# Performance work log

Hardware: AMD Instinct MI355X
Metric: run time of the kernel (lower is better)

The kernel has to match this reference:

```python
import jax, jax.numpy as jnp
import numpy as np

B, S, D = 32, 512, 768
H = 12
HD = D // H
SCALE = HD ** -0.5


def setup_inputs() -> dict:
    key = jax.random.key(0)
    ks = jax.random.split(key, 5)
    return {
        "x": jax.random.normal(ks[0], (B, S, D), dtype=jnp.float32),
        "qkv_w": jax.random.normal(ks[1], (3 * D, D), dtype=jnp.float32) * (D ** -0.5),
        "qkv_b": jax.random.normal(ks[2], (3 * D,), dtype=jnp.float32) * 0.02,
        "proj_w": jax.random.normal(ks[3], (D, D), dtype=jnp.float32) * (D ** -0.5),
        "proj_b": jax.random.normal(ks[4], (D,), dtype=jnp.float32) * 0.02,
    }


def reference(x, qkv_w, qkv_b, proj_w, proj_b) -> jnp.ndarray:
    b, s, d = x.shape
    # fused QKV projection (torch Linear: x @ W.T + b)
    qkv = x @ qkv_w.T + qkv_b                      # [B,S,3D]
    qkv = qkv.reshape(b, s, 3, H, HD)
    qkv = jnp.transpose(qkv, (2, 0, 3, 1, 4))      # [3,B,H,S,HD]
    q, k, v = qkv[0], qkv[1], qkv[2]
    scores = jnp.einsum("bhqd,bhkd->bhqk", q, k) * SCALE  # [B,H,S,S]
    # attn_drop with p=0.0 (eval) -> identity
    attn = jax.nn.softmax(scores, axis=-1)
    out = jnp.einsum("bhqk,bhkd->bhqd", attn, v)   # [B,H,S,HD]
    out = jnp.transpose(out, (0, 2, 1, 3)).reshape(b, s, d)
    out = out @ proj_w.T + proj_b                  # proj_drop p=0.0 -> identity
    return out
```

## Files before the change

kernel.cpp:

```cpp
#include <hip/hip_runtime.h>
#include <hip/hip_bf16.h>

#define B_  32
#define S_  512
#define D_  768
#define H_  12
#define HD_ 64
#define QKV_ELEMS (B_ * H_ * S_ * HD_)

typedef __hip_bfloat16 bf16;
typedef short bf16x8_t __attribute__((ext_vector_type(8)));
typedef float f32x4_t  __attribute__((ext_vector_type(4)));

__device__ __forceinline__ float bf2f(bf16 x) { return __bfloat162float(x); }
__device__ __forceinline__ bf16  f2bf(float x) { return __float2bfloat16(x); }

__device__ __forceinline__ void gl_lds16(const short* g, short* l) {
    __builtin_amdgcn_global_load_lds(
        (const __attribute__((address_space(1))) void*)g,
        (__attribute__((address_space(3))) void*)l, 16, 0, 0);
}

__global__ __launch_bounds__(256) void f2bf3_kernel(
    const float* __restrict__ in0, unsigned short* __restrict__ out0, int n0,
    const float* __restrict__ in1, unsigned short* __restrict__ out1, int n1,
    const float* __restrict__ in2, unsigned short* __restrict__ out2, int n2)
{
    int i = blockIdx.x * 256 + threadIdx.x;
    const float* in; unsigned short* out;
    if (i < n0)           { in = in0; out = out0; }
    else if (i < n0 + n1) { in = in1; out = out1; i -= n0; }
    else                  { in = in2; out = out2; i -= n0 + n1;
                            if (i >= n2) return; }
    float4 v = reinterpret_cast<const float4*>(in)[i];
    ushort4 o;
    o.x = __bfloat16_as_ushort(f2bf(v.x));
    o.y = __bfloat16_as_ushort(f2bf(v.y));
    o.z = __bfloat16_as_ushort(f2bf(v.z));
    o.w = __bfloat16_as_ushort(f2bf(v.w));
    reinterpret_cast<ushort4*>(out)[i] = o;
}

#define GEMM_CORE(As, Bs, Aptr, Bptr, m0, n0, K)                               \
    const int t = threadIdx.x;                                                 \
    const int w = t >> 6, lane = t & 63;                                       \
    const int wr = w >> 1, wc = w & 1;                                         \
    const int quad = lane >> 4, l16 = lane & 15;                               \
    f32x4_t acc[4][4] = {};                                                    \
    const int lrow = lane >> 3;                                                \
    const int scol = (((lane & 7) ^ (lrow & 7)) * 8);                          \
    _Pragma("unroll")                                                          \
    for (int j = 0; j < 4; ++j) {                                              \
        int R = j * 32 + w * 8;                                                \
        gl_lds16((Aptr) + (size_t)((m0) + R + lrow) * (K) + scol, &(As)[R * 64]); \
        gl_lds16((Bptr) + (size_t)((n0) + R + lrow) * (K) + scol, &(Bs)[R * 64]); \
    }                                                                          \
    for (int k0 = 0; k0 < (K); k0 += 64) {                                     \
        __syncthreads();           \
        _Pragma("unroll")                                                      \
        for (int ks = 0; ks < 64; ks += 32) {                                  \
            bf16x8_t af[4], bf_[4];                                            \
            _Pragma("unroll")                                                  \
            for (int tm = 0; tm < 4; ++tm)                                     \
                af[tm] = *(const bf16x8_t*)&(As)[(wr * 64 + tm * 16 + l16) * 64 \
                        + ((((ks >> 3) + quad) ^ (l16 & 7)) * 8)];             \
            _Pragma("unroll")                                                  \
            for (int tn = 0; tn < 4; ++tn)                                     \
                bf_[tn] = *(const bf16x8_t*)&(Bs)[(wc * 64 + tn * 16 + l16) * 64 \
                        + ((((ks >> 3) + quad) ^ (l16 & 7)) * 8)];             \
            _Pragma("unroll")                                                  \
            for (int tm = 0; tm < 4; ++tm)                                     \
                _Pragma("unroll")                                              \
                for (int tn = 0; tn < 4; ++tn)                                 \
                    acc[tm][tn] = __builtin_amdgcn_mfma_f32_16x16x32_bf16(     \
                        af[tm], bf_[tn], acc[tm][tn], 0, 0, 0);                \
        }                                                                      \
        __syncthreads();                   \
        if (k0 + 64 < (K)) {                                                   \
            _Pragma("unroll")                                                  \
            for (int j = 0; j < 4; ++j) {                                      \
                int R = j * 32 + w * 8;                                        \
                gl_lds16((Aptr) + (size_t)((m0) + R + lrow) * (K) + k0 + 64 + scol, \
                         &(As)[R * 64]);                                       \
                gl_lds16((Bptr) + (size_t)((n0) + R + lrow) * (K) + k0 + 64 + scol, \
                         &(Bs)[R * 64]);                                       \
            }                                                                  \
        }                                                                      \
    }

__global__ __launch_bounds__(256, 4) void qkv_gemm_mfma(
    const short* __restrict__ A, const short* __restrict__ W,
    const float* __restrict__ bias,
    bf16* __restrict__ Q, bf16* __restrict__ Kp, bf16* __restrict__ Vp)
{
    __shared__ short As[128 * 64];
    __shared__ short Bs[128 * 64];
    const int bid = blockIdx.x;
    const int swz = (bid & 7) * (2304 / 8) + (bid >> 3);
    const int n0 = (swz % 18) * 128;
    const int m0 = (swz / 18) * 128;
    GEMM_CORE(As, Bs, A, W, m0, n0, 768)

    const int which = n0 / 768;
    const int h = ((n0 + wc * 64) % 768) >> 6;
    bf16* dst = (which == 0) ? Q : (which == 1) ? Kp : Vp;
    float bv[4];
#pragma unroll
    for (int tn = 0; tn < 4; ++tn) bv[tn] = bias[n0 + wc * 64 + tn * 16 + l16];
#pragma unroll
    for (int tm = 0; tm < 4; ++tm) {
#pragma unroll
        for (int r = 0; r < 4; ++r) {
            int m = m0 + wr * 64 + tm * 16 + quad * 4 + r;
            int b = m >> 9, s = m & 511;
            size_t rb = (((size_t)b * H_ + h) * S_ + s) * HD_;
#pragma unroll
            for (int tn = 0; tn < 4; ++tn)
                dst[rb + tn * 16 + l16] = f2bf(acc[tm][tn][r] + bv[tn]);
        }
    }
}

__global__ __launch_bounds__(256, 4) void proj_gemm_mfma(
    const short* __restrict__ A, const short* __restrict__ W,
    const float* __restrict__ bias, float* __restrict__ out)
{
    __shared__ short As[128 * 64];
    __shared__ short Bs[128 * 64];
    const int bid = blockIdx.x;
    const int swz = (bid & 7) * (768 / 8) + (bid >> 3);
    const int n0 = (swz % 6) * 128;
    const int m0 = (swz / 6) * 128;
    GEMM_CORE(As, Bs, A, W, m0, n0, 768)

    float bv[4];
#pragma unroll
    for (int tn = 0; tn < 4; ++tn) bv[tn] = bias[n0 + wc * 64 + tn * 16 + l16];
#pragma unroll
    for (int tm = 0; tm < 4; ++tm) {
#pragma unroll
        for (int r = 0; r < 4; ++r) {
            int m = m0 + wr * 64 + tm * 16 + quad * 4 + r;
#pragma unroll
            for (int tn = 0; tn < 4; ++tn)
                out[(size_t)m * 768 + n0 + wc * 64 + tn * 16 + l16] =
                    acc[tm][tn][r] + bv[tn];
        }
    }
}

#define QT 128
#define KT 64
#define PS 68
#define VS 68

__global__ __launch_bounds__(256, 3) void attn_mfma(
    const short* __restrict__ Qg, const short* __restrict__ Kg,
    const short* __restrict__ Vg, bf16* __restrict__ O)
{
    __shared__ short Ks[2][KT * 64];
    __shared__ short Vt[2][64 * VS];
    __shared__ short Ps[QT * PS];

    const int t = threadIdx.x;
    const int w = t >> 6, lane = t & 63;
    const int quad = lane >> 4, l16 = lane & 15;
    const int lrow = lane >> 3;
    const int scol = (((lane & 7) ^ (lrow & 7)) * 8);
    const int bid = blockIdx.x;
    const int bh = (bid & 7) + 8 * (bid >> 5);
    const int qt = (bid >> 3) & 3;
    const int q0 = qt * QT;
    const size_t base = (size_t)bh * (S_ * HD_);
    const int wq = w * 32;

    bf16x8_t aq[2][2];
#pragma unroll
    for (int tm = 0; tm < 2; ++tm)
#pragma unroll
        for (int ksi = 0; ksi < 2; ++ksi)
            aq[tm][ksi] = *(const bf16x8_t*)(Qg + base
                + (size_t)(q0 + wq + tm * 16 + l16) * 64 + ksi * 32 + quad * 8);

    f32x4_t Oacc[2][4] = {};
    float lsum[2][4] = {};

#pragma unroll
    for (int j = 0; j < 2; ++j) {
        int R = j * 32 + w * 8;
        gl_lds16(Kg + base + (size_t)(R + lrow) * 64 + scol, &Ks[0][R * 64]);
    }
    {
        const bf16x8_t* gv = (const bf16x8_t*)(Vg + base + (size_t)lane * 64 + w * 16);
        bf16x8_t v0 = gv[0], v1 = gv[1];
#pragma unroll
        for (int i = 0; i < 8; ++i) {
            Vt[0][(w * 16 + i) * VS + lane]     = v0[i];
            Vt[0][(w * 16 + 8 + i) * VS + lane] = v1[i];
        }
    }
    __syncthreads();

    for (int kt = 0; kt < 8; ++kt) {
        const int cur = kt & 1, nxt = cur ^ 1;
        bf16x8_t pv0 = {}, pv1 = {};
        if (kt < 7) {
#pragma unroll
            for (int j = 0; j < 2; ++j) {
                int R = j * 32 + w * 8;
                gl_lds16(Kg + base + (size_t)((kt + 1) * KT + R + lrow) * 64 + scol,
                         &Ks[nxt][R * 64]);
            }
            const bf16x8_t* gv = (const bf16x8_t*)(Vg + base
                + (size_t)((kt + 1) * KT + lane) * 64 + w * 16);
            pv0 = gv[0]; pv1 = gv[1];
        }

        f32x4_t sc[2][4] = {};
        __builtin_amdgcn_s_setprio(1);
#pragma unroll
        for (int ks = 0; ks < 64; ks += 32) {
            bf16x8_t bk[4];
#pragma unroll
            for (int tn = 0; tn < 4; ++tn)
                bk[tn] = *(const bf16x8_t*)&Ks[cur][(tn * 16 + l16) * 64
                        + ((((ks >> 3) + quad) ^ (l16 & 7)) * 8)];
#pragma unroll
            for (int tm = 0; tm < 2; ++tm)
#pragma unroll
                for (int tn = 0; tn < 4; ++tn)
                    sc[tm][tn] = __builtin_amdgcn_mfma_f32_16x16x32_bf16(
                        aq[tm][ks >> 5], bk[tn], sc[tm][tn], 0, 0, 0);
        }
        __builtin_amdgcn_s_setprio(0);

#pragma unroll
        for (int tm = 0; tm < 2; ++tm) {
#pragma unroll
            for (int r = 0; r < 4; ++r) {
                int row = wq + tm * 16 + quad * 4 + r;
                float rs = 0.f;
#pragma unroll
                for (int tn = 0; tn < 4; ++tn) {
                    float p = __expf(sc[tm][tn][r] * 0.125f);
                    rs += p;
                    Ps[row * PS + tn * 16 + l16] = (short)__bfloat16_as_ushort(f2bf(p));
                }
                lsum[tm][r] += rs;
            }
        }

        __builtin_amdgcn_s_setprio(1);
#pragma unroll
        for (int ks = 0; ks < 64; ks += 32) {
            bf16x8_t ap[2], bv[4];
#pragma unroll
            for (int tm = 0; tm < 2; ++tm)
                ap[tm] = *(const bf16x8_t*)&Ps[(wq + tm * 16 + l16) * PS + ks + quad * 8];
#pragma unroll
            for (int tn = 0; tn < 4; ++tn)
                bv[tn] = *(const bf16x8_t*)&Vt[cur][(tn * 16 + l16) * VS + ks + quad * 8];
#pragma unroll
            for (int tm = 0; tm < 2; ++tm)
#pragma unroll
                for (int tn = 0; tn < 4; ++tn)
                    Oacc[tm][tn] = __builtin_amdgcn_mfma_f32_16x16x32_bf16(
                        ap[tm], bv[tn], Oacc[tm][tn], 0, 0, 0);
        }
        __builtin_amdgcn_s_setprio(0);

        if (kt < 7) {
#pragma unroll
            for (int i = 0; i < 8; ++i) {
                Vt[nxt][(w * 16 + i) * VS + lane]     = pv0[i];
                Vt[nxt][(w * 16 + 8 + i) * VS + lane] = pv1[i];
            }
        }
        __syncthreads();
    }

    float linv[2][4];
#pragma unroll
    for (int tm = 0; tm < 2; ++tm)
#pragma unroll
        for (int r = 0; r < 4; ++r) {
            float v = lsum[tm][r];
            v += __shfl_xor(v, 1, 64);
            v += __shfl_xor(v, 2, 64);
            v += __shfl_xor(v, 4, 64);
            v += __shfl_xor(v, 8, 64);
            linv[tm][r] = 1.f / v;
        }
    const int b = bh / H_, h = bh % H_;
#pragma unroll
    for (int tm = 0; tm < 2; ++tm) {
#pragma unroll
        for (int r = 0; r < 4; ++r) {
            int row = q0 + wq + tm * 16 + quad * 4 + r;
            size_t ob = ((size_t)b * S_ + row) * D_ + h * HD_;
#pragma unroll
            for (int tn = 0; tn < 4; ++tn)
                O[ob + tn * 16 + l16] = f2bf(Oacc[tm][tn][r] * linv[tm][r]);
        }
    }
}

extern "C" void kernel_launch(void* const* d_in, const int* in_sizes, int n_in,
                              void* d_out, int out_size, void* d_ws, size_t ws_size,
                              hipStream_t stream) {
    const float* x      = (const float*)d_in[0];
    const float* qkv_w  = (const float*)d_in[1];
    const float* qkv_b  = (const float*)d_in[2];
    const float* proj_w = (const float*)d_in[3];
    const float* proj_b = (const float*)d_in[4];
    float* out = (float*)d_out;

    unsigned short* q     = (unsigned short*)d_ws;
    unsigned short* k     = q + QKV_ELEMS;
    unsigned short* v     = k + QKV_ELEMS;
    unsigned short* slot4 = v + QKV_ELEMS;
    unsigned short* wq    = slot4 + QKV_ELEMS;
    unsigned short* wp    = wq + 2304 * 768;

    const int nx = 16384 * 768 / 4, nw1 = 2304 * 768 / 4, nw2 = 768 * 768 / 4;
    f2bf3_kernel<<<(nx + nw1 + nw2 + 255) / 256, 256, 0, stream>>>(
        x, slot4, nx, qkv_w, wq, nw1, proj_w, wp, nw2);

    qkv_gemm_mfma<<<dim3(2304), 256, 0, stream>>>(
        (const short*)slot4, (const short*)wq, qkv_b,
        (bf16*)q, (bf16*)k, (bf16*)v);

    attn_mfma<<<dim3(32 * 12 * 4), 256, 0, stream>>>(
        (const short*)q, (const short*)k, (const short*)v, (bf16*)slot4);

    proj_gemm_mfma<<<dim3(768), 256, 0, stream>>>(
        (const short*)slot4, (const short*)wp, proj_b, out);
}
```

Baseline: 245.3 us.

## Load GEMM weight fragments straight into registers with one-step prefetch, dropping B LDS tile

The shared GEMM core no longer stages the weight (B) tile through LDS. Each wave now loads its B fragments from global memory directly into registers and prefetches the next k-slice while computing the current one. This halves LDS usage and removes the B LDS reads and writes. In exchange each 64-column wave pair re-reads the same weights from global or L2 without sharing, and register pressure rises under launch_bounds(256,4).

```diff
diff --git a/kernel.cpp b/kernel.cpp
--- a/kernel.cpp
+++ b/kernel.cpp
@@ -41,7 +41,7 @@
     reinterpret_cast<ushort4*>(out)[i] = o;
 }
 
-#define GEMM_CORE(As, Bs, Aptr, Bptr, m0, n0, K)                               \
+#define GEMM_CORE(As, Aptr, Bptr, m0, n0, K)                                   \
     const int t = threadIdx.x;                                                 \
     const int w = t >> 6, lane = t & 63;                                       \
     const int wr = w >> 1, wc = w & 1;                                         \
@@ -49,42 +49,60 @@
     f32x4_t acc[4][4] = {};                                                    \
     const int lrow = lane >> 3;                                                \
     const int scol = (((lane & 7) ^ (lrow & 7)) * 8);                          \
+    const short* Bp[4];                                                        \
+    _Pragma("unroll")                                                          \
+    for (int tn = 0; tn < 4; ++tn)                                             \
+        Bp[tn] = (Bptr) + (size_t)((n0) + wc * 64 + tn * 16 + l16) * (K)       \
+                 + quad * 8;                                                   \
     _Pragma("unroll")                                                          \
     for (int j = 0; j < 4; ++j) {                                              \
         int R = j * 32 + w * 8;                                                \
         gl_lds16((Aptr) + (size_t)((m0) + R + lrow) * (K) + scol, &(As)[R * 64]); \
-        gl_lds16((Bptr) + (size_t)((n0) + R + lrow) * (K) + scol, &(Bs)[R * 64]); \
     }                                                                          \
+    bf16x8_t bcur[4][2];                                                       \
+    _Pragma("unroll")                                                          \
+    for (int tn = 0; tn < 4; ++tn)                                             \
+        _Pragma("unroll")                                                      \
+        for (int ks = 0; ks < 2; ++ks)                                         \
+            bcur[tn][ks] = *(const bf16x8_t*)(Bp[tn] + ks * 32);               \
+    _Pragma("unroll")                                                          \
     for (int k0 = 0; k0 < (K); k0 += 64) {                                     \
-        __syncthreads();           \
+        __syncthreads();              \
+        bf16x8_t bnxt[4][2];                                                   \
+        if (k0 + 64 < (K)) {                                                   \
+            _Pragma("unroll")                                                  \
+            for (int tn = 0; tn < 4; ++tn)                                     \
+                _Pragma("unroll")                                              \
+                for (int ks = 0; ks < 2; ++ks)                                 \
+                    bnxt[tn][ks] = *(const bf16x8_t*)(Bp[tn] + k0 + 64 + ks * 32); \
+        }                                                                      \
         _Pragma("unroll")                                                      \
-        for (int ks = 0; ks < 64; ks += 32) {                                  \
-            bf16x8_t af[4], bf_[4];                                            \
+        for (int ks = 0; ks < 2; ++ks) {                                       \
+            bf16x8_t af[4];                                                    \
             _Pragma("unroll")                                                  \
             for (int tm = 0; tm < 4; ++tm)                                     \
                 af[tm] = *(const bf16x8_t*)&(As)[(wr * 64 + tm * 16 + l16) * 64 \
-                        + ((((ks >> 3) + quad) ^ (l16 & 7)) * 8)];             \
-            _Pragma("unroll")                                                  \
-            for (int tn = 0; tn < 4; ++tn)                                     \
-                bf_[tn] = *(const bf16x8_t*)&(Bs)[(wc * 64 + tn * 16 + l16) * 64 \
-                        + ((((ks >> 3) + quad) ^ (l16 & 7)) * 8)];             \
+                        + (((ks * 4 + quad) ^ (l16 & 7)) * 8)];                \
             _Pragma("unroll")                                                  \
             for (int tm = 0; tm < 4; ++tm)                                     \
                 _Pragma("unroll")                                              \
                 for (int tn = 0; tn < 4; ++tn)                                 \
                     acc[tm][tn] = __builtin_amdgcn_mfma_f32_16x16x32_bf16(     \
-                        af[tm], bf_[tn], acc[tm][tn], 0, 0, 0);                \
+                        af[tm], bcur[tn][ks], acc[tm][tn], 0, 0, 0);           \
         }                                                                      \
-        __syncthreads();                   \
+        __syncthreads();           \
         if (k0 + 64 < (K)) {                                                   \
             _Pragma("unroll")                                                  \
             for (int j = 0; j < 4; ++j) {                                      \
                 int R = j * 32 + w * 8;                                        \
                 gl_lds16((Aptr) + (size_t)((m0) + R + lrow) * (K) + k0 + 64 + scol, \
                          &(As)[R * 64]);                                       \
-                gl_lds16((Bptr) + (size_t)((n0) + R + lrow) * (K) + k0 + 64 + scol, \
-                         &(Bs)[R * 64]);                                       \
             }                                                                  \
+            _Pragma("unroll")                                                  \
+            for (int tn = 0; tn < 4; ++tn)                                     \
+                _Pragma("unroll")                                              \
+                for (int ks = 0; ks < 2; ++ks)                                 \
+                    bcur[tn][ks] = bnxt[tn][ks];                               \
         }                                                                      \
     }
 
@@ -94,12 +112,11 @@
     bf16* __restrict__ Q, bf16* __restrict__ Kp, bf16* __restrict__ Vp)
 {
     __shared__ short As[128 * 64];
-    __shared__ short Bs[128 * 64];
     const int bid = blockIdx.x;
     const int swz = (bid & 7) * (2304 / 8) + (bid >> 3);
     const int n0 = (swz % 18) * 128;
     const int m0 = (swz / 18) * 128;
-    GEMM_CORE(As, Bs, A, W, m0, n0, 768)
+    GEMM_CORE(As, A, W, m0, n0, 768)
 
     const int which = n0 / 768;
     const int h = ((n0 + wc * 64) % 768) >> 6;
@@ -126,12 +143,11 @@
     const float* __restrict__ bias, float* __restrict__ out)
 {
     __shared__ short As[128 * 64];
-    __shared__ short Bs[128 * 64];
     const int bid = blockIdx.x;
     const int swz = (bid & 7) * (768 / 8) + (bid >> 3);
     const int n0 = (swz % 6) * 128;
     const int m0 = (swz / 6) * 128;
-    GEMM_CORE(As, Bs, A, W, m0, n0, 768)
+    GEMM_CORE(As, A, W, m0, n0, 768)
 
     float bv[4];
 #pragma unroll
```

Result: slower. 329.1 us (+34.2%).

## Split attention block into 8 waves with 16 query rows each

Applied to the files above, without the earlier changes.

The attention kernel now launches 512 threads per block, and each of 8 waves owns 16 query rows instead of 32, which halves the per-wave accumulators and Q fragments. K/V tile loading is redistributed so each wave loads 8 rows of K and an 8-column slice of V. The aim is lower register pressure and more resident waves to hide latency. In exchange, each K/V LDS fragment is reused across fewer MFMAs per wave, and block-wide syncs now involve more waves.

```diff
diff --git a/kernel.cpp b/kernel.cpp
--- a/kernel.cpp
+++ b/kernel.cpp
@@ -154,7 +154,7 @@
 #define PS 68
 #define VS 68
 
-__global__ __launch_bounds__(256, 3) void attn_mfma(
+__global__ __launch_bounds__(512, 4) void attn_mfma(
     const short* __restrict__ Qg, const short* __restrict__ Kg,
     const short* __restrict__ Vg, bf16* __restrict__ O)
 {
@@ -172,51 +172,37 @@
     const int qt = (bid >> 3) & 3;
     const int q0 = qt * QT;
     const size_t base = (size_t)bh * (S_ * HD_);
-    const int wq = w * 32;
-
-    bf16x8_t aq[2][2];
-#pragma unroll
-    for (int tm = 0; tm < 2; ++tm)
-#pragma unroll
-        for (int ksi = 0; ksi < 2; ++ksi)
-            aq[tm][ksi] = *(const bf16x8_t*)(Qg + base
-                + (size_t)(q0 + wq + tm * 16 + l16) * 64 + ksi * 32 + quad * 8);
-
-    f32x4_t Oacc[2][4] = {};
-    float lsum[2][4] = {};
-
-#pragma unroll
-    for (int j = 0; j < 2; ++j) {
-        int R = j * 32 + w * 8;
-        gl_lds16(Kg + base + (size_t)(R + lrow) * 64 + scol, &Ks[0][R * 64]);
-    }
+    const int wq = w * 16;
+
+    bf16x8_t aq[2];
+#pragma unroll
+    for (int ksi = 0; ksi < 2; ++ksi)
+        aq[ksi] = *(const bf16x8_t*)(Qg + base
+            + (size_t)(q0 + wq + l16) * 64 + ksi * 32 + quad * 8);
+
+    f32x4_t Oacc[4] = {};
+    float lsum[4] = {};
+
+    gl_lds16(Kg + base + (size_t)(w * 8 + lrow) * 64 + scol, &Ks[0][w * 8 * 64]);
     {
-        const bf16x8_t* gv = (const bf16x8_t*)(Vg + base + (size_t)lane * 64 + w * 16);
-        bf16x8_t v0 = gv[0], v1 = gv[1];
-#pragma unroll
-        for (int i = 0; i < 8; ++i) {
-            Vt[0][(w * 16 + i) * VS + lane]     = v0[i];
-            Vt[0][(w * 16 + 8 + i) * VS + lane] = v1[i];
-        }
+        bf16x8_t v0 = *(const bf16x8_t*)(Vg + base + (size_t)lane * 64 + w * 8);
+#pragma unroll
+        for (int i = 0; i < 8; ++i)
+            Vt[0][(w * 8 + i) * VS + lane] = v0[i];
     }
     __syncthreads();
 
     for (int kt = 0; kt < 8; ++kt) {
         const int cur = kt & 1, nxt = cur ^ 1;
-        bf16x8_t pv0 = {}, pv1 = {};
+        bf16x8_t pv = {};
         if (kt < 7) {
-#pragma unroll
-            for (int j = 0; j < 2; ++j) {
-                int R = j * 32 + w * 8;
-                gl_lds16(Kg + base + (size_t)((kt + 1) * KT + R + lrow) * 64 + scol,
-                         &Ks[nxt][R * 64]);
-            }
-            const bf16x8_t* gv = (const bf16x8_t*)(Vg + base
-                + (size_t)((kt + 1) * KT + lane) * 64 + w * 16);
-            pv0 = gv[0]; pv1 = gv[1];
-        }
-
-        f32x4_t sc[2][4] = {};
+            gl_lds16(Kg + base + (size_t)((kt + 1) * KT + w * 8 + lrow) * 64 + scol,
+                     &Ks[nxt][w * 8 * 64]);
+            pv = *(const bf16x8_t*)(Vg + base
+                + (size_t)((kt + 1) * KT + lane) * 64 + w * 8);
+        }
+
+        f32x4_t sc[4] = {};
         __builtin_amdgcn_s_setprio(1);
 #pragma unroll
         for (int ks = 0; ks < 64; ks += 32) {
@@ -226,82 +212,66 @@
                 bk[tn] = *(const bf16x8_t*)&Ks[cur][(tn * 16 + l16) * 64
                         + ((((ks >> 3) + quad) ^ (l16 & 7)) * 8)];
 #pragma unroll
-            for (int tm = 0; tm < 2; ++tm)
-#pragma unroll
-                for (int tn = 0; tn < 4; ++tn)
-                    sc[tm][tn] = __builtin_amdgcn_mfma_f32_16x16x32_bf16(
-                        aq[tm][ks >> 5], bk[tn], sc[tm][tn], 0, 0, 0);
+            for (int tn = 0; tn < 4; ++tn)
+                sc[tn] = __builtin_amdgcn_mfma_f32_16x16x32_bf16(
+                    aq[ks >> 5], bk[tn], sc[tn], 0, 0, 0);
         }
         __builtin_amdgcn_s_setprio(0);
 
 #pragma unroll
-        for (int tm = 0; tm < 2; ++tm) {
-#pragma unroll
-            for (int r = 0; r < 4; ++r) {
-                int row = wq + tm * 16 + quad * 4 + r;
-                float rs = 0.f;
-#pragma unroll
-                for (int tn = 0; tn < 4; ++tn) {
-                    float p = __expf(sc[tm][tn][r] * 0.125f);
-                    rs += p;
-                    Ps[row * PS + tn * 16 + l16] = (short)__bfloat16_as_ushort(f2bf(p));
-                }
-                lsum[tm][r] += rs;
+        for (int r = 0; r < 4; ++r) {
+            int row = wq + quad * 4 + r;
+            float rs = 0.f;
+#pragma unroll
+            for (int tn = 0; tn < 4; ++tn) {
+                float p = __expf(sc[tn][r] * 0.125f);
+                rs += p;
+                Ps[row * PS + tn * 16 + l16] = (short)__bfloat16_as_ushort(f2bf(p));
             }
+            lsum[r] += rs;
         }
 
         __builtin_amdgcn_s_setprio(1);
 #pragma unroll
         for (int ks = 0; ks < 64; ks += 32) {
-            bf16x8_t ap[2], bv[4];
-#pragma unroll
-            for (int tm = 0; tm < 2; ++tm)
-                ap[tm] = *(const bf16x8_t*)&Ps[(wq + tm * 16 + l16) * PS + ks + quad * 8];
+            bf16x8_t ap, bv[4];
+            ap = *(const bf16x8_t*)&Ps[(wq + l16) * PS + ks + quad * 8];
 #pragma unroll
             for (int tn = 0; tn < 4; ++tn)
                 bv[tn] = *(const bf16x8_t*)&Vt[cur][(tn * 16 + l16) * VS + ks + quad * 8];
 #pragma unroll
-            for (int tm = 0; tm < 2; ++tm)
-#pragma unroll
-                for (int tn = 0; tn < 4; ++tn)
-                    Oacc[tm][tn] = __builtin_amdgcn_mfma_f32_16x16x32_bf16(
-                        ap[tm], bv[tn], Oacc[tm][tn], 0, 0, 0);
+            for (int tn = 0; tn < 4; ++tn)
+                Oacc[tn] = __builtin_amdgcn_mfma_f32_16x16x32_bf16(
+                    ap, bv[tn], Oacc[tn], 0, 0, 0);
         }
         __builtin_amdgcn_s_setprio(0);
 
         if (kt < 7) {
 #pragma unroll
-            for (int i = 0; i < 8; ++i) {
-                Vt[nxt][(w * 16 + i) * VS + lane]     = pv0[i];
-                Vt[nxt][(w * 16 + 8 + i) * VS + lane] = pv1[i];
-            }
+            for (int i = 0; i < 8; ++i)
+                Vt[nxt][(w * 8 + i) * VS + lane] = pv[i];
         }
         __syncthreads();
     }
 
-    float linv[2][4];
-#pragma unroll
-    for (int tm = 0; tm < 2; ++tm)
-#pragma unroll
-        for (int r = 0; r < 4; ++r) {
-            float v = lsum[tm][r];
-            v += __shfl_xor(v, 1, 64);
-            v += __shfl_xor(v, 2, 64);
-            v += __shfl_xor(v, 4, 64);
-            v += __shfl_xor(v, 8, 64);
-            linv[tm][r] = 1.f / v;
-        }
+    float linv[4];
+#pragma unroll
+    for (int r = 0; r < 4; ++r) {
+        float v = lsum[r];
+        v += __shfl_xor(v, 1, 64);
+        v += __shfl_xor(v, 2, 64);
+        v += __shfl_xor(v, 4, 64);
+        v += __shfl_xor(v, 8, 64);
+        linv[r] = 1.f / v;
+    }
     const int b = bh / H_, h = bh % H_;
 #pragma unroll
-    for (int tm = 0; tm < 2; ++tm) {
-#pragma unroll
-        for (int r = 0; r < 4; ++r) {
-            int row = q0 + wq + tm * 16 + quad * 4 + r;
-            size_t ob = ((size_t)b * S_ + row) * D_ + h * HD_;
-#pragma unroll
-            for (int tn = 0; tn < 4; ++tn)
-                O[ob + tn * 16 + l16] = f2bf(Oacc[tm][tn][r] * linv[tm][r]);
-        }
+    for (int r = 0; r < 4; ++r) {
+        int row = q0 + wq + quad * 4 + r;
+        size_t ob = ((size_t)b * S_ + row) * D_ + h * HD_;
+#pragma unroll
+        for (int tn = 0; tn < 4; ++tn)
+            O[ob + tn * 16 + l16] = f2bf(Oacc[tn][r] * linv[r]);
     }
 }
 
@@ -330,7 +300,7 @@
         (const short*)slot4, (const short*)wq, qkv_b,
         (bf16*)q, (bf16*)k, (bf16*)v);
 
-    attn_mfma<<<dim3(32 * 12 * 4), 256, 0, stream>>>(
+    attn_mfma<<<dim3(32 * 12 * 4), 512, 0, stream>>>(
         (const short*)q, (const short*)k, (const short*)v, (bf16*)slot4);
 
     proj_gemm_mfma<<<dim3(768), 256, 0, stream>>>(
```

New measurement: 239.3 us. 2.5% less time.
